# Kernel tuning notes

Measured on AMD Instinct MI355X. Metric: run time of the kernel, lower is better.

Reference implementation:

```python
import jax, jax.numpy as jnp
import numpy as np

B, S, H = 4, 1024, 1024
R = 512          # num_rules
M = 1024         # memory_size
HEADS = 16
STEPS = 3        # inference_steps
TEMP = 1.0       # softmax_temperature
LN_EPS = 1e-5


def setup_inputs() -> dict:
    key = jax.random.key(0)
    ks = jax.random.split(key, 40)
    std = 0.02
    p = lambda k, shp: (jax.random.normal(k, shp, jnp.float32) * std)
    inp = {
        "hidden_states": jax.random.normal(ks[0], (B, S, H), jnp.float32),
        "rule_embeddings": p(ks[1], (R, H)),
        "rule_sel_w": p(ks[2], (H, R)), "rule_sel_b": jnp.zeros((R,), jnp.float32),
        # self-attention (nn.MultiheadAttention) projections
        "attn_wq": p(ks[3], (H, H)), "attn_bq": jnp.zeros((H,), jnp.float32),
        "attn_wk": p(ks[4], (H, H)), "attn_bk": jnp.zeros((H,), jnp.float32),
        "attn_wv": p(ks[5], (H, H)), "attn_bv": jnp.zeros((H,), jnp.float32),
        "attn_wo": p(ks[6], (H, H)), "attn_bo": jnp.zeros((H,), jnp.float32),
        # memory bank + key/query/value projections
        "memory": p(ks[7], (M, H)),
        "mem_q_w": p(ks[8], (H, H)), "mem_q_b": jnp.zeros((H,), jnp.float32),
        "mem_k_w": p(ks[9], (H, H)), "mem_k_b": jnp.zeros((H,), jnp.float32),
        "mem_v_w": p(ks[10], (H, H)), "mem_v_b": jnp.zeros((H,), jnp.float32),
        # memory_attention (nn.MultiheadAttention) projections
        "mattn_wq": p(ks[11], (H, H)), "mattn_bq": jnp.zeros((H,), jnp.float32),
        "mattn_wk": p(ks[12], (H, H)), "mattn_bk": jnp.zeros((H,), jnp.float32),
        "mattn_wv": p(ks[13], (H, H)), "mattn_bv": jnp.zeros((H,), jnp.float32),
        "mattn_wo": p(ks[14], (H, H)), "mattn_bo": jnp.zeros((H,), jnp.float32),
        # rule_application: Linear(2H,H)+LN+GELU+Linear(H,H)
        "ra_w1": p(ks[15], (2 * H, H)), "ra_b1": jnp.zeros((H,), jnp.float32),
        "ra_ln_s": jnp.ones((H,), jnp.float32), "ra_ln_b": jnp.zeros((H,), jnp.float32),
        "ra_w2": p(ks[16], (H, H)), "ra_b2": jnp.zeros((H,), jnp.float32),
        # confidence_scorer
        "conf_w": p(ks[17], (H, 1)), "conf_b": jnp.zeros((1,), jnp.float32),
    }
    return inp


def _mha(q_in, k_in, v_in, wq, bq, wk, bk, wv, bv, wo, bo):
    # standard nn.MultiheadAttention math (batch_first, eval mode -> no dropout)
    b, sq, h = q_in.shape
    d = h // HEADS
    qh = (q_in @ wq + bq).reshape(b, sq, HEADS, d)
    kh = (k_in @ wk + bk).reshape(b, -1, HEADS, d)
    vh = (v_in @ wv + bv).reshape(b, -1, HEADS, d)
    scores = jnp.einsum('bqhd,bkhd->bhqk', qh, kh) / jnp.sqrt(jnp.asarray(d, qh.dtype))
    probs = jax.nn.softmax(scores, axis=-1)
    out = jnp.einsum('bhqk,bkhd->bqhd', probs, vh).reshape(b, sq, h)
    return out @ wo + bo


def _ln(x, s, b):
    mu = x.mean(-1, keepdims=True)
    var = ((x - mu) ** 2).mean(-1, keepdims=True)
    return (x - mu) / jnp.sqrt(var + LN_EPS) * s + b


def reference(hidden_states, rule_embeddings, rule_sel_w, rule_sel_b,
              attn_wq, attn_bq, attn_wk, attn_bk, attn_wv, attn_bv, attn_wo, attn_bo,
              memory, mem_q_w, mem_q_b, mem_k_w, mem_k_b, mem_v_w, mem_v_b,
              mattn_wq, mattn_bq, mattn_wk, mattn_bk, mattn_wv, mattn_bv, mattn_wo, mattn_bo,
              ra_w1, ra_b1, ra_ln_s, ra_ln_b, ra_w2, ra_b2, conf_w, conf_b):
    h = hidden_states
    b = h.shape[0]
    # memory keys/values are input-independent: project once, broadcast over batch
    mk = jnp.broadcast_to((memory @ mem_k_w + mem_k_b)[None], (b, M, H))
    mv = jnp.broadcast_to((memory @ mem_v_w + mem_v_b)[None], (b, M, H))
    for _ in range(STEPS):
        # rule routing: soft selection over the rule-embedding table
        rule_probs = jax.nn.softmax((h @ rule_sel_w + rule_sel_b) / TEMP, axis=-1)  # [B,S,R]
        selected = jnp.einsum('bsr,rh->bsh', rule_probs, rule_embeddings)           # [B,S,H]
        # self-attention reasoning
        h = h + _mha(h, h, h, attn_wq, attn_bq, attn_wk, attn_bk,
                     attn_wv, attn_bv, attn_wo, attn_bo)
        # memory attention
        mq = h @ mem_q_w + mem_q_b
        h = h + _mha(mq, mk, mv, mattn_wq, mattn_bq, mattn_wk, mattn_bk,
                     mattn_wv, mattn_bv, mattn_wo, mattn_bo)
        # rule application MLP on [h ; selected_rules]
        x = jnp.concatenate([h, selected], axis=-1)                                  # [B,S,2H]
        u = jax.nn.gelu(_ln(x @ ra_w1 + ra_b1, ra_ln_s, ra_ln_b), approximate=False)
        h = h + (u @ ra_w2 + ra_b2)
    confidence = jax.nn.sigmoid(h @ conf_w + conf_b)  # [B,S,1]
    return h, confidence
```

## Files before the change

### kernel.cpp

```cpp
#include <hip/hip_runtime.h>
#include <stdint.h>

typedef _Float16 f16;
typedef __attribute__((ext_vector_type(4))) float floatx4;
typedef __attribute__((ext_vector_type(8))) f16   f16x8;
typedef __attribute__((ext_vector_type(4))) f16   f16x4;

#define GLD_LDS16(gp, lp)                                                                      \
  __builtin_amdgcn_global_load_lds((const __attribute__((address_space(1))) void*)(uintptr_t)(gp), \
                                   (__attribute__((address_space(3))) void*)(uintptr_t)(lp), 16, 0, 0)

struct SrlOut {
  int n0;
  const float* bias;
  const float* resid;
  float* Cf; f16* Cb;
  int ldcf, ldcb, transV;
  long long sCb, sCh;
};
struct SrlGemmArgs {
  const f16* A; const f16* B;
  int M, N, K, lda, ldb;
  long long sAb, sAh, sBb, sBh;
  float alpha;
  int nOuts;
  SrlOut out[4];
};

template<int BM, int BN, int MINW>
__global__ __launch_bounds__(256, MINW) void srl_gemm(SrlGemmArgs g) {
  constexpr int BK = 64;
  constexpr int ACH = BM / 32;
  constexpr int BCH = BN / 32;
  constexpr int MI  = (BM == 128 && BN == 128) ? 4 : 2;
  constexpr int NI  = (BN == 128) ? 4 : ((BM == 128) ? 4 : 2);
  __shared__ f16 As[BM * BK];
  __shared__ f16 Bs[BN * BK];
  const int tid  = threadIdx.x;
  const int wid  = tid >> 6;
  const int lane = tid & 63;
  const int z  = blockIdx.z, zh = z & 15, zb = z >> 4;

  const int gx = gridDim.x;
  const int NT = gx * gridDim.y;
  const int L  = blockIdx.y * gx + blockIdx.x;
  const int W  = ((NT & 7) == 0) ? ((L & 7) * (NT >> 3) + (L >> 3)) : L;
  const int tn = (W % gx) * BN;
  const int tm = (W / gx) * BM;

  const f16* Ab = g.A + (long long)zb * g.sAb + (long long)zh * g.sAh + (long long)tm * g.lda;
  const f16* Bb = g.B + (long long)zb * g.sBb + (long long)zh * g.sBh + (long long)tn * g.ldb;
  const int maxAr = g.M - 1 - tm;
  const int maxBr = g.N - 1 - tn;

  int aR[ACH], aO[ACH];
#pragma unroll
  for (int i = 0; i < ACH; ++i) {
    int e = wid * (BM * 16) + i * 512 + lane * 8;
    int r = e >> 6, s = (e >> 3) & 7;
    aR[i] = r; aO[i] = ((s - r) & 7) * 8;
  }
  int bR[BCH], bO[BCH];
#pragma unroll
  for (int i = 0; i < BCH; ++i) {
    int e = wid * (BN * 16) + i * 512 + lane * 8;
    int r = e >> 6, s = (e >> 3) & 7;
    bR[i] = r; bO[i] = ((s - r) & 7) * 8;
  }
  f16* lA = As + wid * (BM * 16);
  f16* lB = Bs + wid * (BN * 16);

  floatx4 acc[MI][NI];
#pragma unroll
  for (int a = 0; a < MI; ++a)
#pragma unroll
    for (int b = 0; b < NI; ++b) {
      acc[a][b][0] = 0.f; acc[a][b][1] = 0.f; acc[a][b][2] = 0.f; acc[a][b][3] = 0.f;
    }

  const int wm = (BM == 128 && BN == 128) ? (wid & 1) * 64
               : (BN == 128)              ? 0
               : (BM == 128)              ? wid * 32
                                          : (wid & 1) * 32;
  const int wn = (BM == 128 && BN == 128) ? (wid >> 1) * 64
               : (BM == 64 && BN == 64)   ? (wid >> 1) * 32
                                          : 0;
  const int lm = lane & 15;
  const int quad = lane >> 4;

  for (int k0 = 0; k0 < g.K; k0 += BK) {
    __syncthreads();
#pragma unroll
    for (int i = 0; i < ACH; ++i) {
      int r = aR[i] <= maxAr ? aR[i] : maxAr;
      GLD_LDS16(Ab + (long long)r * g.lda + (k0 + aO[i]), lA + i * 512);
    }
#pragma unroll
    for (int i = 0; i < BCH; ++i) {
      int r = bR[i] <= maxBr ? bR[i] : maxBr;
      GLD_LDS16(Bb + (long long)r * g.ldb + (k0 + bO[i]), lB + i * 512);
    }
    __syncthreads();
#pragma unroll
    for (int ks = 0; ks < 2; ++ks) {
      f16x8 af[MI], bfr[NI];
#pragma unroll
      for (int mi = 0; mi < MI; ++mi) {
        int row = wm + mi * 16 + lm;
        int sg = ((ks * 4 + quad) + row) & 7;
        af[mi] = *(const f16x8*)(As + row * 64 + sg * 8);
      }
#pragma unroll
      for (int ni = 0; ni < NI; ++ni) {
        int row = wn + ni * 16 + lm;
        int sg = ((ks * 4 + quad) + row) & 7;
        bfr[ni] = *(const f16x8*)(Bs + row * 64 + sg * 8);
      }
#pragma unroll
      for (int mi = 0; mi < MI; ++mi)
#pragma unroll
        for (int ni = 0; ni < NI; ++ni)
          acc[mi][ni] = __builtin_amdgcn_mfma_f32_16x16x32_f16(af[mi], bfr[ni], acc[mi][ni], 0, 0, 0);
    }
  }

  int oi = 0;
  for (int j = 1; j < g.nOuts; ++j)
    if (tn >= g.out[j].n0) oi = j;
  const SrlOut O = g.out[oi];
  const long long zc = (long long)zb * O.sCb + (long long)zh * O.sCh;
#pragma unroll
  for (int mi = 0; mi < MI; ++mi) {
#pragma unroll
    for (int r = 0; r < 4; ++r) {
      int m = tm + wm + mi * 16 + quad * 4 + r;
      if (m >= g.M) continue;
#pragma unroll
      for (int ni = 0; ni < NI; ++ni) {
        int n = tn + wn + ni * 16 + lm;
        if (n >= g.N) continue;
        int nl = n - O.n0;
        float v = acc[mi][ni][r] * g.alpha;
        if (O.bias)  v += O.bias[nl];
        if (O.resid) v += O.resid[(long long)m * O.ldcf + nl];
        if (O.Cf)    O.Cf[zc + (long long)m * O.ldcf + nl] = v;
        if (O.Cb) {
          long long idx = O.transV
              ? ((long long)(m >> 10) * 1048576 + (long long)nl * 1024 + (m & 1023))
              : (zc + (long long)m * O.ldcb + nl);
          O.Cb[idx] = (f16)v;
        }
      }
    }
  }
}

__global__ __launch_bounds__(512, 4) void srl_gemm_p(SrlGemmArgs g) {
  __shared__ f16 As[2][8192];
  __shared__ f16 Bs[2][8192];
  const int tid  = threadIdx.x;
  const int wid  = tid >> 6;
  const int lane = tid & 63;

  const int gx  = gridDim.x;
  const int NTt = gx * gridDim.y;
  const int L   = blockIdx.y * gx + blockIdx.x;
  const int W   = ((NTt & 7) == 0) ? ((L & 7) * (NTt >> 3) + (L >> 3)) : L;
  const int tn  = (W % gx) * 128;
  const int tm  = (W / gx) * 128;

  const f16* Ab = g.A + (long long)tm * g.lda;
  const f16* Bb = g.B + (long long)tn * g.ldb;

  int aR[2], aO[2];
#pragma unroll
  for (int i = 0; i < 2; ++i) {
    int e = wid * 1024 + i * 512 + lane * 8;
    int r = e >> 6, s = (e >> 3) & 7;
    aR[i] = r; aO[i] = ((s - r) & 7) * 8;
  }

  const int wm = (wid >> 1) * 32;
  const int wn = (wid & 1) * 64;
  const int lm = lane & 15;
  const int quad = lane >> 4;

  floatx4 acc[2][4];
#pragma unroll
  for (int a = 0; a < 2; ++a)
#pragma unroll
    for (int b = 0; b < 4; ++b) {
      acc[a][b][0] = 0.f; acc[a][b][1] = 0.f; acc[a][b][2] = 0.f; acc[a][b][3] = 0.f;
    }

  const int nk = g.K >> 6;

  auto stage = [&](int kt, int bsel) {
    const int k0 = kt << 6;
    f16* lA = &As[bsel][0] + wid * 1024;
    f16* lB = &Bs[bsel][0] + wid * 1024;
#pragma unroll
    for (int i = 0; i < 2; ++i)
      GLD_LDS16(Ab + (long long)aR[i] * g.lda + (k0 + aO[i]), lA + i * 512);
#pragma unroll
    for (int i = 0; i < 2; ++i)
      GLD_LDS16(Bb + (long long)aR[i] * g.ldb + (k0 + aO[i]), lB + i * 512);
  };

  stage(0, 0);
  asm volatile("s_waitcnt vmcnt(0)" ::: "memory");
  __builtin_amdgcn_s_barrier();

  auto onestep = [&](int t, int cb) {
    if (t + 1 < nk) stage(t + 1, cb ^ 1);
    asm volatile("" ::: "memory");
    const f16* Asb = &As[cb][0];
    const f16* Bsb = &Bs[cb][0];
#pragma unroll
    for (int ks = 0; ks < 2; ++ks) {
      f16x8 af[2], bfr[4];
#pragma unroll
      for (int mi = 0; mi < 2; ++mi) {
        int row = wm + mi * 16 + lm;
        int sg = ((ks * 4 + quad) + row) & 7;
        af[mi] = *(const f16x8*)(Asb + row * 64 + sg * 8);
      }
#pragma unroll
      for (int ni = 0; ni < 4; ++ni) {
        int row = wn + ni * 16 + lm;
        int sg = ((ks * 4 + quad) + row) & 7;
        bfr[ni] = *(const f16x8*)(Bsb + row * 64 + sg * 8);
      }
#pragma unroll
      for (int mi = 0; mi < 2; ++mi)
#pragma unroll
        for (int ni = 0; ni < 4; ++ni)
          acc[mi][ni] = __builtin_amdgcn_mfma_f32_16x16x32_f16(af[mi], bfr[ni], acc[mi][ni], 0, 0, 0);
    }
    asm volatile("s_waitcnt vmcnt(0) lgkmcnt(0)" ::: "memory");
    __builtin_amdgcn_s_barrier();
  };

  for (int t = 0; t < nk; t += 2) {
    onestep(t, 0);
    onestep(t + 1, 1);
  }

  int oi = 0;
  for (int j = 1; j < g.nOuts; ++j)
    if (tn >= g.out[j].n0) oi = j;
  const SrlOut O = g.out[oi];
#pragma unroll
  for (int mi = 0; mi < 2; ++mi) {
#pragma unroll
    for (int r = 0; r < 4; ++r) {
      int m = tm + wm + mi * 16 + quad * 4 + r;
#pragma unroll
      for (int ni = 0; ni < 4; ++ni) {
        int n = tn + wn + ni * 16 + lm;
        int nl = n - O.n0;
        float v = acc[mi][ni][r] * g.alpha;
        if (O.bias)  v += O.bias[nl];
        if (O.resid) v += O.resid[(long long)m * O.ldcf + nl];
        if (O.Cf)    O.Cf[(long long)m * O.ldcf + nl] = v;
        if (O.Cb) {
          long long idx = O.transV
              ? ((long long)(m >> 10) * 1048576 + (long long)nl * 1024 + (m & 1023))
              : ((long long)m * O.ldcb + nl);
          O.Cb[idx] = (f16)v;
        }
      }
    }
  }
}

struct SrlFlashArgs {
  const f16* Q; const f16* K; const f16* VT; f16* O;
  long long sQb, sKb, sVb;
  float scale;
};

__global__ __launch_bounds__(256, 2) void srl_flash(SrlFlashArgs a) {
  __shared__ f16 Qs[8192];
  __shared__ f16 Ks[8192];
  __shared__ f16 VTs[8192];
  __shared__ f16 Ps[4][4096];
  const int tid = threadIdx.x, wid = tid >> 6, lane = tid & 63;
  const int quad = lane >> 4, c = lane & 15;
  const int L = blockIdx.x;
  const int bh = (L & 7) + ((L >> 6) << 3);
  const int qt = (L >> 3) & 7;
  const int b = bh >> 4, h = bh & 15;
  const f16* Qg = a.Q + (long long)b * a.sQb + (long long)qt * 131072 + h * 64;
  const f16* Kg = a.K + (long long)b * a.sKb + h * 64;
  const f16* Vg = a.VT + (long long)b * a.sVb + (long long)h * 65536;
  f16* Og = a.O + (long long)b * 1048576 + (long long)qt * 131072 + h * 64;

  int rRow[4], rOff[4];
#pragma unroll
  for (int i = 0; i < 4; ++i) {
    int e = wid * 2048 + i * 512 + lane * 8;
    int r = e >> 6, gL = (e >> 3) & 7;
    rRow[i] = r; rOff[i] = ((gL - r) & 7) * 8;
  }
  int vRow[4], vOff[4];
#pragma unroll
  for (int i = 0; i < 4; ++i) {
    int e = wid * 2048 + i * 512 + lane * 8;
    int d = e >> 7, gL = (e >> 3) & 15;
    vRow[i] = d; vOff[i] = ((gL - (d & 7)) & 15) * 8;
  }

#pragma unroll
  for (int i = 0; i < 4; ++i)
    GLD_LDS16(Qg + (long long)rRow[i] * 1024 + rOff[i], Qs + wid * 2048 + i * 512);

  f16x8 kreg[4], vreg[4];
#pragma unroll
  for (int i = 0; i < 4; ++i)
    kreg[i] = *(const f16x8*)(Kg + (long long)rRow[i] * 1024 + rOff[i]);
#pragma unroll
  for (int i = 0; i < 4; ++i)
    vreg[i] = *(const f16x8*)(Vg + (long long)vRow[i] * 1024 + vOff[i]);
#pragma unroll
  for (int i = 0; i < 4; ++i)
    *(f16x8*)(Ks + wid * 2048 + i * 512 + lane * 8) = kreg[i];
#pragma unroll
  for (int i = 0; i < 4; ++i)
    *(f16x8*)(VTs + wid * 2048 + i * 512 + lane * 8) = vreg[i];
  __syncthreads();

  const int wq = wid * 32;
  f16x8 qf[2][2];
#pragma unroll
  for (int nf = 0; nf < 2; ++nf)
#pragma unroll
    for (int ch = 0; ch < 2; ++ch) {
      int row = wq + nf * 16 + c;
      int slot = ((ch * 4 + quad) + row) & 7;
      f16x8 v = *(const f16x8*)(Qs + row * 64 + slot * 8);
      f16 sc = (f16)a.scale;
#pragma unroll
      for (int j = 0; j < 8; ++j) v[j] = v[j] * sc;
      qf[nf][ch] = v;
    }

  float l_s[2] = {0.f, 0.f};
  floatx4 Oa[2][4];
#pragma unroll
  for (int nf = 0; nf < 2; ++nf)
#pragma unroll
    for (int no = 0; no < 4; ++no) {
      Oa[nf][no][0] = 0.f; Oa[nf][no][1] = 0.f; Oa[nf][no][2] = 0.f; Oa[nf][no][3] = 0.f;
    }

  for (int t = 0; t < 8; ++t) {
    if (t < 7) {
#pragma unroll
      for (int i = 0; i < 4; ++i)
        kreg[i] = *(const f16x8*)(Kg + (long long)((t + 1) * 128 + rRow[i]) * 1024 + rOff[i]);
#pragma unroll
      for (int i = 0; i < 4; ++i)
        vreg[i] = *(const f16x8*)(Vg + (long long)vRow[i] * 1024 + ((t + 1) * 128 + vOff[i]));
    }

    floatx4 sT[2][8];
#pragma unroll
    for (int nf = 0; nf < 2; ++nf)
#pragma unroll
      for (int mf = 0; mf < 8; ++mf) {
        sT[nf][mf][0] = 0.f; sT[nf][mf][1] = 0.f; sT[nf][mf][2] = 0.f; sT[nf][mf][3] = 0.f;
      }
    __builtin_amdgcn_s_setprio(1);
#pragma unroll
    for (int ch = 0; ch < 2; ++ch)
#pragma unroll
      for (int mf = 0; mf < 8; ++mf) {
        int key = mf * 16 + c;
        int slot = ((ch * 4 + quad) + key) & 7;
        f16x8 kf = *(const f16x8*)(Ks + key * 64 + slot * 8);
        sT[0][mf] = __builtin_amdgcn_mfma_f32_16x16x32_f16(kf, qf[0][ch], sT[0][mf], 0, 0, 0);
        sT[1][mf] = __builtin_amdgcn_mfma_f32_16x16x32_f16(kf, qf[1][ch], sT[1][mf], 0, 0, 0);
      }
    __builtin_amdgcn_s_setprio(0);

#pragma unroll
    for (int nf = 0; nf < 2; ++nf) {
      float lt = 0.f;
      const int q = nf * 16 + c;
#pragma unroll
      for (int mf = 0; mf < 8; ++mf) {
        f16x4 pk;
#pragma unroll
        for (int r = 0; r < 4; ++r) {
          float p = __builtin_amdgcn_exp2f(sT[nf][mf][r]);
          lt += p;
          pk[r] = (f16)p;
        }
        int kg = mf * 2 + (quad >> 1), sub = (quad & 1) * 4;
        int slot = (kg + (q & 7)) & 15;
        *(f16x4*)(Ps[wid] + q * 128 + slot * 8 + sub) = pk;
      }
      lt += __shfl_xor(lt, 16);
      lt += __shfl_xor(lt, 32);
      l_s[nf] += lt;
    }
#pragma unroll
    for (int cc = 0; cc < 4; ++cc) {
      f16x8 af[2];
#pragma unroll
      for (int nf = 0; nf < 2; ++nf) {
        int q = nf * 16 + c;
        int slot = ((cc * 4 + quad) + (q & 7)) & 15;
        af[nf] = *(const f16x8*)(Ps[wid] + q * 128 + slot * 8);
      }
      __builtin_amdgcn_s_setprio(1);
#pragma unroll
      for (int no = 0; no < 4; ++no) {
        int d = no * 16 + c;
        int slot = ((cc * 4 + quad) + (d & 7)) & 15;
        f16x8 vf = *(const f16x8*)(VTs + d * 128 + slot * 8);
        Oa[0][no] = __builtin_amdgcn_mfma_f32_16x16x32_f16(af[0], vf, Oa[0][no], 0, 0, 0);
        Oa[1][no] = __builtin_amdgcn_mfma_f32_16x16x32_f16(af[1], vf, Oa[1][no], 0, 0, 0);
      }
      __builtin_amdgcn_s_setprio(0);
    }

    if (t < 7) {
      __syncthreads();
#pragma unroll
      for (int i = 0; i < 4; ++i)
        *(f16x8*)(Ks + wid * 2048 + i * 512 + lane * 8) = kreg[i];
#pragma unroll
      for (int i = 0; i < 4; ++i)
        *(f16x8*)(VTs + wid * 2048 + i * 512 + lane * 8) = vreg[i];
      __syncthreads();
    }
  }

#pragma unroll
  for (int nf = 0; nf < 2; ++nf)
#pragma unroll
    for (int r = 0; r < 4; ++r) {
      float li = 1.f / __shfl(l_s[nf], quad * 4 + r);
      int qrow = wq + nf * 16 + quad * 4 + r;
#pragma unroll
      for (int no = 0; no < 4; ++no)
        Qs[qrow * 64 + no * 16 + c] = (f16)(Oa[nf][no][r] * li);
    }
  __syncthreads();
#pragma unroll
  for (int i = 0; i < 4; ++i) {
    int e = wid * 2048 + i * 512 + lane * 8;
    int row = e >> 6, col = e & 63;
    *(f16x8*)(Og + (long long)row * 1024 + col) = *(const f16x8*)(Qs + e);
  }
}

__global__ __launch_bounds__(256) void srl_softmax_rule(const float* logits, f16* probs) {
  __shared__ float red[16];
  const long long row = blockIdx.x;
  const float* p = logits + row * 512;
  const int tid = threadIdx.x;
  float v0 = p[tid], v1 = p[tid + 256];
  float mx = fmaxf(v0, v1);
#pragma unroll
  for (int o = 32; o > 0; o >>= 1) mx = fmaxf(mx, __shfl_down(mx, o));
  const int wid = tid >> 6, lane = tid & 63;
  if (lane == 0) red[wid] = mx;
  __syncthreads();
  if (tid == 0) red[8] = fmaxf(fmaxf(red[0], red[1]), fmaxf(red[2], red[3]));
  __syncthreads();
  mx = red[8];
  float e0 = __expf(v0 - mx), e1 = __expf(v1 - mx);
  float s = e0 + e1;
#pragma unroll
  for (int o = 32; o > 0; o >>= 1) s += __shfl_down(s, o);
  if (lane == 0) red[wid + 4] = s;
  __syncthreads();
  if (tid == 0) red[9] = 1.f / (red[4] + red[5] + red[6] + red[7]);
  __syncthreads();
  const float inv = red[9];
  probs[row * 512 + tid] = (f16)(e0 * inv);
  probs[row * 512 + tid + 256] = (f16)(e1 * inv);
}

__global__ __launch_bounds__(256) void srl_ln_gelu(const float* x, const float* gam, const float* bet, f16* out) {
  __shared__ float red[16];
  const long long row = blockIdx.x;
  const float* p = x + row * 1024;
  const int tid = threadIdx.x;
  float4 xv = *(const float4*)(p + tid * 4);
  float v[4] = {xv.x, xv.y, xv.z, xv.w};
  float s = v[0] + v[1] + v[2] + v[3];
  float s2 = v[0] * v[0] + v[1] * v[1] + v[2] * v[2] + v[3] * v[3];
#pragma unroll
  for (int o = 32; o > 0; o >>= 1) { s += __shfl_down(s, o); s2 += __shfl_down(s2, o); }
  const int wid = tid >> 6, lane = tid & 63;
  if (lane == 0) { red[wid] = s; red[wid + 4] = s2; }
  __syncthreads();
  if (tid == 0) {
    float ts = red[0] + red[1] + red[2] + red[3];
    float ts2 = red[4] + red[5] + red[6] + red[7];
    float mu = ts * (1.f / 1024.f);
    float var = ts2 * (1.f / 1024.f) - mu * mu;
    red[8] = mu;
    red[9] = rsqrtf(var + 1e-5f);
  }
  __syncthreads();
  const float mu = red[8], rstd = red[9];
  f16x4 o4;
#pragma unroll
  for (int i = 0; i < 4; ++i) {
    int c = tid * 4 + i;
    float t = (v[i] - mu) * rstd * gam[c] + bet[c];
    float ge = 0.5f * t * (1.f + erff(t * 0.70710678118654752f));
    o4[i] = (f16)ge;
  }
  *(f16x4*)(out + row * 1024 + tid * 4) = o4;
}

struct SrlTcEnt { const float* src; f16* dst; int rows, cols, trans, tileStart; };
struct SrlTcArgs { SrlTcEnt e[16]; };

__global__ __launch_bounds__(256) void srl_convert_weights(SrlTcArgs a) {
  __shared__ float t[32][33];
  const int bt = blockIdx.x;
  int ei = 0;
#pragma unroll
  for (int j = 1; j < 16; ++j)
    if (bt >= a.e[j].tileStart) ei = j;
  SrlTcEnt E = a.e[ei];
  const int lt = bt - E.tileStart;
  const int tcols = E.cols >> 5;
  const int tr = lt / tcols;
  const int tc = lt - tr * tcols;
  const int r = threadIdx.x >> 5;
  const int c = threadIdx.x & 31;
  if (!E.trans) {
#pragma unroll
    for (int p = 0; p < 4; ++p) {
      long long rr = tr * 32 + r + p * 8;
      long long idx = rr * E.cols + tc * 32 + c;
      E.dst[idx] = (f16)E.src[idx];
    }
  } else {
#pragma unroll
    for (int p = 0; p < 4; ++p)
      t[r + p * 8][c] = E.src[(long long)(tr * 32 + r + p * 8) * E.cols + tc * 32 + c];
    __syncthreads();
#pragma unroll
    for (int p = 0; p < 4; ++p)
      E.dst[(long long)(tc * 32 + r + p * 8) * E.rows + tr * 32 + c] = (f16)t[c][r + p * 8];
  }
}

__global__ __launch_bounds__(256) void srl_prep_bias(const float* rsel_b, const float* bq,
                                                     const float* bk, const float* bv,
                                                     const float* bmq, const float* maq_w,
                                                     const float* bmaq,
                                                     float* bias_qkvr, float* bcomp) {
  int i = blockIdx.x * 256 + threadIdx.x;
  if (i < 3584) {
    float v;
    if (i < 512) v = rsel_b[i];
    else if (i < 1536) v = bq[i - 512];
    else if (i < 2560) v = bk[i - 1536];
    else v = bv[i - 2560];
    bias_qkvr[i] = v;
  } else if (i < 3584 + 1024) {
    int m = i - 3584;
    float s = bmaq[m];
    for (int t = 0; t < 1024; ++t) s += bmq[t] * maq_w[(long long)t * 1024 + m];
    bcomp[m] = s;
  }
}

__global__ __launch_bounds__(256) void srl_h_init(const float* hidden, float* hf, f16* hx) {
  long long base = ((long long)blockIdx.x * 256 + threadIdx.x) * 4;
  float4 v = *(const float4*)(hidden + base);
  *(float4*)(hf + base) = v;
  long long row = base >> 10;
  int col = (int)(base & 1023);
  f16x4 b;
  b[0] = (f16)v.x; b[1] = (f16)v.y; b[2] = (f16)v.z; b[3] = (f16)v.w;
  *(f16x4*)(hx + row * 2048 + col) = b;
}

__global__ __launch_bounds__(256) void srl_finalize(const float* hf, const float* w, const float* b,
                                                    float* out, float* conf) {
  const int bid = blockIdx.x;
  if (bid < 4096) {
    long long base = ((long long)bid * 256 + threadIdx.x) * 4;
    *(float4*)(out + base) = *(const float4*)(hf + base);
  } else {
    const int row = (bid - 4096) * 4 + (threadIdx.x >> 6);
    const int lane = threadIdx.x & 63;
    const float* p = hf + (long long)row * 1024;
    float s = 0.f;
    for (int j = lane; j < 1024; j += 64) s += p[j] * w[j];
#pragma unroll
    for (int o = 32; o > 0; o >>= 1) s += __shfl_down(s, o);
    if (lane == 0) conf[row] = 1.f / (1.f + __expf(-(s + b[0])));
  }
}

extern "C" void kernel_launch(void* const* d_in, const int* in_sizes, int n_in,
                              void* d_out, int out_size, void* d_ws, size_t ws_size,
                              hipStream_t stream) {
  (void)in_sizes; (void)n_in; (void)out_size; (void)ws_size;
  const float* in_hidden   = (const float*)d_in[0];
  const float* in_rule_emb = (const float*)d_in[1];
  const float* in_rsel_w   = (const float*)d_in[2];
  const float* in_rsel_b   = (const float*)d_in[3];
  const float* in_attn_wq  = (const float*)d_in[4];
  const float* in_attn_bq  = (const float*)d_in[5];
  const float* in_attn_wk  = (const float*)d_in[6];
  const float* in_attn_bk  = (const float*)d_in[7];
  const float* in_attn_wv  = (const float*)d_in[8];
  const float* in_attn_bv  = (const float*)d_in[9];
  const float* in_attn_wo  = (const float*)d_in[10];
  const float* in_attn_bo  = (const float*)d_in[11];
  const float* in_memory   = (const float*)d_in[12];
  const float* in_mq_w     = (const float*)d_in[13];
  const float* in_mq_b     = (const float*)d_in[14];
  const float* in_mk_w     = (const float*)d_in[15];
  const float* in_mk_b     = (const float*)d_in[16];
  const float* in_mv_w     = (const float*)d_in[17];
  const float* in_mv_b     = (const float*)d_in[18];
  const float* in_maq_w    = (const float*)d_in[19];
  const float* in_maq_b    = (const float*)d_in[20];
  const float* in_mak_w    = (const float*)d_in[21];
  const float* in_mak_b    = (const float*)d_in[22];
  const float* in_mav_w    = (const float*)d_in[23];
  const float* in_mav_b    = (const float*)d_in[24];
  const float* in_mao_w    = (const float*)d_in[25];
  const float* in_mao_b    = (const float*)d_in[26];
  const float* in_ra_w1    = (const float*)d_in[27];
  const float* in_ra_b1    = (const float*)d_in[28];
  const float* in_ln_s     = (const float*)d_in[29];
  const float* in_ln_b     = (const float*)d_in[30];
  const float* in_ra_w2    = (const float*)d_in[31];
  const float* in_ra_b2    = (const float*)d_in[32];
  const float* in_conf_w   = (const float*)d_in[33];
  const float* in_conf_b   = (const float*)d_in[34];

  char* ws = (char*)d_ws;
  size_t off = 0;
  auto alloc = [&](size_t bytes) -> void* {
    void* p = ws + off;
    off = (off + bytes + 255) & ~(size_t)255;
    return p;
  };
  f16* wt_qkvr    = (f16*)alloc(3584 * 1024 * 2);
  float* bias_qkvr= (float*)alloc(3584 * 4);
  f16* wt_attn_o  = (f16*)alloc(1048576 * 2);
  f16* wt_mq_comp = (f16*)alloc(1048576 * 2);
  float* bcomp    = (float*)alloc(1024 * 4);
  f16* wt_mattn_o = (f16*)alloc(1048576 * 2);
  f16* wt_ra1     = (f16*)alloc(2097152 * 2);
  f16* wt_ra2     = (f16*)alloc(1048576 * 2);
  f16* wt_remb    = (f16*)alloc(524288 * 2);
  f16* wt_mem_kv  = (f16*)alloc(2097152 * 2);
  f16* wt_mattn_k = (f16*)alloc(1048576 * 2);
  f16* wt_mattn_v = (f16*)alloc(1048576 * 2);
  f16* mem_h      = (f16*)alloc(1048576 * 2);
  f16* mk_h       = (f16*)alloc(1048576 * 2);
  f16* mv_h       = (f16*)alloc(1048576 * 2);
  f16* mak_h      = (f16*)alloc(1048576 * 2);
  f16* mavT_h     = (f16*)alloc(1048576 * 2);
  float* h_f      = (float*)alloc(4194304 * 4);
  f16* hx         = (f16*)alloc(8388608 * 2);
  f16* q_h        = (f16*)alloc(4194304 * 2);
  f16* k_h        = (f16*)alloc(4194304 * 2);
  f16* vT_h       = (f16*)alloc(4194304 * 2);
  f16* ctx_h      = (f16*)alloc(4194304 * 2);
  f16* u_h        = (f16*)alloc(4194304 * 2);
  char* arena     = (char*)alloc(16777216);
  float* logits_f = (float*)arena;
  f16* probs_h    = (f16*)(arena + 8388608);
  float* ra1_f    = (float*)arena;
  f16* mqw_nt     = (f16*)arena;
  f16* wmaq_t     = (f16*)(arena + 2097152);

  auto mkOut = [](int n0, const float* bias, const float* resid, float* Cf, int ldcf,
                  f16* Cb, int ldcb, int transV, long long sCb, long long sCh) {
    SrlOut o;
    o.n0 = n0; o.bias = bias; o.resid = resid; o.Cf = Cf; o.Cb = Cb;
    o.ldcf = ldcf; o.ldcb = ldcb; o.transV = transV; o.sCb = sCb; o.sCh = sCh;
    return o;
  };
  auto runP = [&](int M, int N, int K, const f16* A, int lda, const f16* B, int ldb,
                  float alpha, SrlGemmArgs g) {
    g.A = A; g.B = B; g.M = M; g.N = N; g.K = K; g.lda = lda; g.ldb = ldb;
    g.sAb = 0; g.sAh = 0; g.sBb = 0; g.sBh = 0; g.alpha = alpha;
    dim3 grid(N / 128, M / 128, 1);
    hipLaunchKernelGGL(srl_gemm_p, grid, dim3(512), 0, stream, g);
  };
  auto runS = [&](int M, int N, int K, const f16* A, int lda, const f16* B, int ldb,
                  float alpha, const float* bias, const float* resid, float* Cf, int ldcf,
                  f16* Cb, int ldcb, int transV) {
    SrlGemmArgs g{};
    g.nOuts = 1;
    g.out[0] = mkOut(0, bias, resid, Cf, ldcf, Cb, ldcb, transV, 0, 0);
    g.A = A; g.B = B; g.M = M; g.N = N; g.K = K; g.lda = lda; g.ldb = ldb;
    g.sAb = 0; g.sAh = 0; g.sBb = 0; g.sBh = 0; g.alpha = alpha;
    dim3 grid((N + 63) / 64, (M + 63) / 64, 1);
    hipLaunchKernelGGL((srl_gemm<64, 64, 4>), grid, dim3(256), 0, stream, g);
  };
  auto runSm = [&](int M, int N, int K, const f16* A, int lda, const f16* B, int ldb,
                   float alpha, SrlGemmArgs g) {
    g.A = A; g.B = B; g.M = M; g.N = N; g.K = K; g.lda = lda; g.ldb = ldb;
    g.sAb = 0; g.sAh = 0; g.sBb = 0; g.sBh = 0; g.alpha = alpha;
    dim3 grid((N + 63) / 64, (M + 63) / 64, 1);
    hipLaunchKernelGGL((srl_gemm<64, 64, 4>), grid, dim3(256), 0, stream, g);
  };

  SrlTcArgs tc;
  int ts = 0;
  auto setent = [&](int i, const float* s, f16* d, int rows, int cols, int trans) {
    tc.e[i].src = s; tc.e[i].dst = d; tc.e[i].rows = rows; tc.e[i].cols = cols;
    tc.e[i].trans = trans; tc.e[i].tileStart = ts;
    ts += (rows / 32) * (cols / 32);
  };
  setent(0,  in_attn_wq, wt_qkvr + 512 * 1024, 1024, 1024, 1);
  setent(1,  in_attn_wk, wt_qkvr + 1536 * 1024, 1024, 1024, 1);
  setent(2,  in_attn_wv, wt_qkvr + 2560 * 1024, 1024, 1024, 1);
  setent(3,  in_rsel_w,  wt_qkvr, 1024, 512, 1);
  setent(4,  in_attn_wo, wt_attn_o, 1024, 1024, 1);
  setent(5,  in_mq_w,    mqw_nt, 1024, 1024, 0);
  setent(6,  in_maq_w,   wmaq_t, 1024, 1024, 1);
  setent(7,  in_mak_w,   wt_mattn_k, 1024, 1024, 1);
  setent(8,  in_mav_w,   wt_mattn_v, 1024, 1024, 1);
  setent(9,  in_mk_w,    wt_mem_kv, 1024, 1024, 1);
  setent(10, in_mv_w,    wt_mem_kv + 1048576, 1024, 1024, 1);
  setent(11, in_mao_w,   wt_mattn_o, 1024, 1024, 1);
  setent(12, in_ra_w1,   wt_ra1, 2048, 1024, 1);
  setent(13, in_ra_w2,   wt_ra2, 1024, 1024, 1);
  setent(14, in_rule_emb, wt_remb, 512, 1024, 1);
  setent(15, in_memory,  mem_h, 1024, 1024, 0);
  hipLaunchKernelGGL(srl_convert_weights, dim3(ts), dim3(256), 0, stream, tc);
  hipLaunchKernelGGL(srl_prep_bias, dim3(18), dim3(256), 0, stream,
                     in_rsel_b, in_attn_bq, in_attn_bk, in_attn_bv,
                     in_mq_b, in_maq_w, in_maq_b, bias_qkvr, bcomp);
  hipLaunchKernelGGL(srl_h_init, dim3(4096), dim3(256), 0, stream, in_hidden, h_f, hx);

  {
    SrlGemmArgs g{};
    g.nOuts = 2;
    g.out[0] = mkOut(0, in_mk_b, nullptr, nullptr, 0, mk_h, 1024, 0, 0, 0);
    g.out[1] = mkOut(1024, in_mv_b, nullptr, nullptr, 0, mv_h, 1024, 0, 0, 0);
    runSm(1024, 2048, 1024, mem_h, 1024, wt_mem_kv, 1024, 1.f, g);
  }
  runS(1024, 1024, 1024, mk_h, 1024, wt_mattn_k, 1024, 1.f, in_mak_b, nullptr, nullptr, 0, mak_h, 1024, 0);
  runS(1024, 1024, 1024, mv_h, 1024, wt_mattn_v, 1024, 1.f, in_mav_b, nullptr, nullptr, 0, mavT_h, 0, 1);
  runS(1024, 1024, 1024, wmaq_t, 1024, mqw_nt, 1024, 1.f, nullptr, nullptr, nullptr, 0, wt_mq_comp, 1024, 0);

  const float kLog2e = 1.4426950408889634f;
  for (int step = 0; step < 3; ++step) {
    {
      SrlGemmArgs g{};
      g.nOuts = 4;
      g.out[0] = mkOut(0,    bias_qkvr,        nullptr, logits_f, 512, nullptr, 0, 0, 0, 0);
      g.out[1] = mkOut(512,  bias_qkvr + 512,  nullptr, nullptr, 0, q_h, 1024, 0, 0, 0);
      g.out[2] = mkOut(1536, bias_qkvr + 1536, nullptr, nullptr, 0, k_h, 1024, 0, 0, 0);
      g.out[3] = mkOut(2560, bias_qkvr + 2560, nullptr, nullptr, 0, vT_h, 0, 1, 0, 0);
      runP(4096, 3584, 1024, hx, 2048, wt_qkvr, 1024, 1.f, g);
    }
    hipLaunchKernelGGL(srl_softmax_rule, dim3(4096), dim3(256), 0, stream, logits_f, probs_h);
    runS(4096, 1024, 512, probs_h, 512, wt_remb, 512, 1.f, nullptr, nullptr, nullptr, 0, hx + 1024, 2048, 0);
    {
      SrlFlashArgs fa;
      fa.Q = q_h; fa.K = k_h; fa.VT = vT_h; fa.O = ctx_h;
      fa.sQb = 1048576; fa.sKb = 1048576; fa.sVb = 1048576; fa.scale = 0.125f * kLog2e;
      hipLaunchKernelGGL(srl_flash, dim3(512), dim3(256), 0, stream, fa);
    }
    runS(4096, 1024, 1024, ctx_h, 1024, wt_attn_o, 1024, 1.f, in_attn_bo, h_f, h_f, 1024, hx, 2048, 0);
    runS(4096, 1024, 1024, hx, 2048, wt_mq_comp, 1024, 1.f, bcomp, nullptr, nullptr, 0, k_h, 1024, 0);
    {
      SrlFlashArgs fa;
      fa.Q = k_h; fa.K = mak_h; fa.VT = mavT_h; fa.O = ctx_h;
      fa.sQb = 1048576; fa.sKb = 0; fa.sVb = 0; fa.scale = 0.125f * kLog2e;
      hipLaunchKernelGGL(srl_flash, dim3(512), dim3(256), 0, stream, fa);
    }
    runS(4096, 1024, 1024, ctx_h, 1024, wt_mattn_o, 1024, 1.f, in_mao_b, h_f, h_f, 1024, hx, 2048, 0);
    runS(4096, 1024, 2048, hx, 2048, wt_ra1, 2048, 1.f, in_ra_b1, nullptr, ra1_f, 1024, nullptr, 0, 0);
    hipLaunchKernelGGL(srl_ln_gelu, dim3(4096), dim3(256), 0, stream, ra1_f, in_ln_s, in_ln_b, u_h);
    runS(4096, 1024, 1024, u_h, 1024, wt_ra2, 1024, 1.f, in_ra_b2, h_f, h_f, 1024, hx, 2048, 0);
  }

  hipLaunchKernelGGL(srl_finalize, dim3(5120), dim3(256), 0, stream, h_f, in_conf_w, in_conf_b,
                     (float*)d_out, (float*)d_out + 4194304);
}
```

Before: 1.045 ms.

## Register-prefetch next K tile in srl_gemm and specialize to 64x64 non-batched tiles

Replaces the synchronous global_load_lds staging in srl_gemm with a register-staged software pipeline: the next K tile is loaded into registers while MFMAs run on the current LDS tile, then written to LDS between barriers. It also hardcodes the warp layout to 2x2 fragments (64x64 tiles) and removes batch/head z-offsets, narrowing the kernel to non-batched 64x64 use. This aims to hide global load latency, at the cost of extra registers and VGPR-to-LDS writes. Any caller still using other tile shapes or a z grid would break.

```diff
diff --git a/kernel.cpp b/kernel.cpp
--- a/kernel.cpp
+++ b/kernel.cpp
@@ -32,14 +32,13 @@
   constexpr int BK = 64;
   constexpr int ACH = BM / 32;
   constexpr int BCH = BN / 32;
-  constexpr int MI  = (BM == 128 && BN == 128) ? 4 : 2;
-  constexpr int NI  = (BN == 128) ? 4 : ((BM == 128) ? 4 : 2);
+  constexpr int MI  = 2;
+  constexpr int NI  = 2;
   __shared__ f16 As[BM * BK];
   __shared__ f16 Bs[BN * BK];
   const int tid  = threadIdx.x;
   const int wid  = tid >> 6;
   const int lane = tid & 63;
-  const int z  = blockIdx.z, zh = z & 15, zb = z >> 4;
 
   const int gx = gridDim.x;
   const int NT = gx * gridDim.y;
@@ -48,8 +47,8 @@
   const int tn = (W % gx) * BN;
   const int tm = (W / gx) * BM;
 
-  const f16* Ab = g.A + (long long)zb * g.sAb + (long long)zh * g.sAh + (long long)tm * g.lda;
-  const f16* Bb = g.B + (long long)zb * g.sBb + (long long)zh * g.sBh + (long long)tn * g.ldb;
+  const f16* Ab = g.A + (long long)tm * g.lda;
+  const f16* Bb = g.B + (long long)tn * g.ldb;
   const int maxAr = g.M - 1 - tm;
   const int maxBr = g.N - 1 - tn;
 
@@ -58,14 +57,16 @@
   for (int i = 0; i < ACH; ++i) {
     int e = wid * (BM * 16) + i * 512 + lane * 8;
     int r = e >> 6, s = (e >> 3) & 7;
-    aR[i] = r; aO[i] = ((s - r) & 7) * 8;
+    aR[i] = (r <= maxAr) ? r : maxAr;
+    aO[i] = ((s - r) & 7) * 8;
   }
   int bR[BCH], bO[BCH];
 #pragma unroll
   for (int i = 0; i < BCH; ++i) {
     int e = wid * (BN * 16) + i * 512 + lane * 8;
     int r = e >> 6, s = (e >> 3) & 7;
-    bR[i] = r; bO[i] = ((s - r) & 7) * 8;
+    bR[i] = (r <= maxBr) ? r : maxBr;
+    bO[i] = ((s - r) & 7) * 8;
   }
   f16* lA = As + wid * (BM * 16);
   f16* lB = Bs + wid * (BN * 16);
@@ -78,29 +79,37 @@
       acc[a][b][0] = 0.f; acc[a][b][1] = 0.f; acc[a][b][2] = 0.f; acc[a][b][3] = 0.f;
     }
 
-  const int wm = (BM == 128 && BN == 128) ? (wid & 1) * 64
-               : (BN == 128)              ? 0
-               : (BM == 128)              ? wid * 32
-                                          : (wid & 1) * 32;
-  const int wn = (BM == 128 && BN == 128) ? (wid >> 1) * 64
-               : (BM == 64 && BN == 64)   ? (wid >> 1) * 32
-                                          : 0;
+  const int wm = (wid & 1) * 32;
+  const int wn = (wid >> 1) * 32;
   const int lm = lane & 15;
   const int quad = lane >> 4;
 
-  for (int k0 = 0; k0 < g.K; k0 += BK) {
-    __syncthreads();
-#pragma unroll
-    for (int i = 0; i < ACH; ++i) {
-      int r = aR[i] <= maxAr ? aR[i] : maxAr;
-      GLD_LDS16(Ab + (long long)r * g.lda + (k0 + aO[i]), lA + i * 512);
-    }
-#pragma unroll
-    for (int i = 0; i < BCH; ++i) {
-      int r = bR[i] <= maxBr ? bR[i] : maxBr;
-      GLD_LDS16(Bb + (long long)r * g.ldb + (k0 + bO[i]), lB + i * 512);
-    }
-    __syncthreads();
+  f16x8 aReg[ACH], bReg[BCH];
+#pragma unroll
+  for (int i = 0; i < ACH; ++i)
+    aReg[i] = *(const f16x8*)(Ab + (long long)aR[i] * g.lda + aO[i]);
+#pragma unroll
+  for (int i = 0; i < BCH; ++i)
+    bReg[i] = *(const f16x8*)(Bb + (long long)bR[i] * g.ldb + bO[i]);
+#pragma unroll
+  for (int i = 0; i < ACH; ++i)
+    *(f16x8*)(lA + i * 512 + lane * 8) = aReg[i];
+#pragma unroll
+  for (int i = 0; i < BCH; ++i)
+    *(f16x8*)(lB + i * 512 + lane * 8) = bReg[i];
+  __syncthreads();
+
+  const int nk = g.K / BK;
+  for (int t = 0; t < nk; ++t) {
+    if (t + 1 < nk) {
+      const int k0 = (t + 1) * BK;
+#pragma unroll
+      for (int i = 0; i < ACH; ++i)
+        aReg[i] = *(const f16x8*)(Ab + (long long)aR[i] * g.lda + (k0 + aO[i]));
+#pragma unroll
+      for (int i = 0; i < BCH; ++i)
+        bReg[i] = *(const f16x8*)(Bb + (long long)bR[i] * g.ldb + (k0 + bO[i]));
+    }
 #pragma unroll
     for (int ks = 0; ks < 2; ++ks) {
       f16x8 af[MI], bfr[NI];
@@ -122,13 +131,22 @@
         for (int ni = 0; ni < NI; ++ni)
           acc[mi][ni] = __builtin_amdgcn_mfma_f32_16x16x32_f16(af[mi], bfr[ni], acc[mi][ni], 0, 0, 0);
     }
+    if (t + 1 < nk) {
+      __syncthreads();
+#pragma unroll
+      for (int i = 0; i < ACH; ++i)
+        *(f16x8*)(lA + i * 512 + lane * 8) = aReg[i];
+#pragma unroll
+      for (int i = 0; i < BCH; ++i)
+        *(f16x8*)(lB + i * 512 + lane * 8) = bReg[i];
+      __syncthreads();
+    }
   }
 
   int oi = 0;
   for (int j = 1; j < g.nOuts; ++j)
     if (tn >= g.out[j].n0) oi = j;
   const SrlOut O = g.out[oi];
-  const long long zc = (long long)zb * O.sCb + (long long)zh * O.sCh;
 #pragma unroll
   for (int mi = 0; mi < MI; ++mi) {
 #pragma unroll
@@ -143,11 +161,11 @@
         float v = acc[mi][ni][r] * g.alpha;
         if (O.bias)  v += O.bias[nl];
         if (O.resid) v += O.resid[(long long)m * O.ldcf + nl];
-        if (O.Cf)    O.Cf[zc + (long long)m * O.ldcf + nl] = v;
+        if (O.Cf)    O.Cf[(long long)m * O.ldcf + nl] = v;
         if (O.Cb) {
           long long idx = O.transV
               ? ((long long)(m >> 10) * 1048576 + (long long)nl * 1024 + (m & 1023))
-              : (zc + (long long)m * O.ldcb + nl);
+              : ((long long)m * O.ldcb + nl);
           O.Cb[idx] = (f16)v;
         }
       }
```

Result: slower. 1.162 ms (+11.3%).
